# Optimization experiments

Hardware: AMD Instinct MI355X
Metric: run time of the kernel (lower is better)

Reference implementation:

```python
import jax, jax.numpy as jnp
import numpy as np

B, S, D = 2, 4096, 2048
H = 16
DN, DR = 128, 64          # qk_nope_head_dim, qk_rope_head_dim
DQK = DN + DR             # 192
DV = 128                  # v_head_dim
QL, KVL = 512, 512        # q_lora_rank, kv_lora_rank
L = 64                    # block_len
SCALE = DQK ** -0.5
ROPE_THETA = 10000.0


def rms_norm(x, w, eps=1e-6):
    x = x.astype(jnp.float32)
    return x * jax.lax.rsqrt(jnp.mean(x * x, axis=-1, keepdims=True) + eps) * w


def apply_rope(x, cos, sin):
    # x: [b, s, h, d]; cos/sin: [s, d//2]; pairs are consecutive (view(-1,2))
    shp = x.shape
    x2 = x.reshape(shp[:-1] + (-1, 2))
    xr, xi = x2[..., 0], x2[..., 1]
    c = cos[None, :, None, :]
    s_ = sin[None, :, None, :]
    yr = xr * c - xi * s_
    yi = xr * s_ + xi * c
    return jnp.stack([yr, yi], axis=-1).reshape(shp)


def ssa(q, k, v, init_state):
    # chunked causal linear attention; q,k: [b,s,h,dk], v: [b,s,h,dv]
    b, s, h, dk = q.shape
    dv = v.shape[-1]
    nc = s // L
    qc = q.reshape(b, nc, L, h, dk)
    kc = k.reshape(b, nc, L, h, dk)
    vc = v.reshape(b, nc, L, h, dv)
    # per-chunk k^T v outer products -> [b,c,h,dk,dv]
    kv = jnp.einsum('bclhk,bclhv->bchkv', kc, vc)
    cs = jnp.cumsum(kv, axis=1)
    # exclusive prefix (state at chunk start) + initial state
    states = jnp.concatenate([jnp.zeros_like(cs[:, :1]), cs[:, :-1]], axis=1) + init_state[:, None]
    inter = jnp.einsum('bclhk,bchkv->bclhv', qc, states)
    sc = jnp.einsum('bclhk,bcmhk->bchlm', qc, kc)
    mask = jnp.tril(jnp.ones((L, L), dtype=bool))
    sc = jnp.where(mask, sc, 0.0)
    intra = jnp.einsum('bchlm,bcmhv->bclhv', sc, vc)
    return (inter + intra).reshape(b, s, h, dv)


def setup_inputs() -> dict:
    key = jax.random.key(0)
    ks = jax.random.split(key, 8)
    x = jax.random.normal(ks[0], (B, S, D), dtype=jnp.float32)
    # rope tables for qk_rope_head_dim
    inv = 1.0 / (ROPE_THETA ** (np.arange(0, DR, 2, dtype=np.float32) / DR))
    ang = np.outer(np.arange(S, dtype=np.float32), inv)
    cos = jnp.asarray(np.cos(ang), dtype=jnp.float32)
    sin = jnp.asarray(np.sin(ang), dtype=jnp.float32)
    std = 0.02
    wq_a = jax.random.normal(ks[1], (QL, D), dtype=jnp.float32) * std
    wq_b = jax.random.normal(ks[2], (H * DQK, QL), dtype=jnp.float32) * std
    wkv_a = jax.random.normal(ks[3], (KVL + DR, D), dtype=jnp.float32) * std
    wkv_b = jax.random.normal(ks[4], (H * (DN + DV), KVL), dtype=jnp.float32) * std
    wo = jax.random.normal(ks[5], (D, H * DV), dtype=jnp.float32) * std
    q_norm_w = jnp.ones((QL,), dtype=jnp.float32)
    kv_norm_w = jnp.ones((KVL,), dtype=jnp.float32)
    init_state = jnp.zeros((B, H, DQK, DV), dtype=jnp.float32)
    return {"x": x, "start_pos": 0, "cos": cos, "sin": sin,
            "wq_a": wq_a, "wq_b": wq_b, "wkv_a": wkv_a, "wkv_b": wkv_b,
            "wo": wo, "q_norm_w": q_norm_w, "kv_norm_w": kv_norm_w,
            "init_state": init_state}


def reference(x, start_pos, cos, sin, wq_a, wq_b, wkv_a, wkv_b, wo,
              q_norm_w, kv_norm_w, init_state):
    b, s, _ = x.shape
    q = rms_norm(x @ wq_a.T, q_norm_w) @ wq_b.T
    q = q.reshape(b, s, H, DQK)
    q_nope, q_pe = q[..., :DN], q[..., DN:]
    q_pe = apply_rope(q_pe, cos, sin)
    kvp = x @ wkv_a.T
    kv_lat, k_pe = kvp[..., :KVL], kvp[..., KVL:]
    k_pe = apply_rope(k_pe[:, :, None, :], cos, sin)  # [b,s,1,DR]
    kv = rms_norm(kv_lat, kv_norm_w) @ wkv_b.T
    kv = kv.reshape(b, s, H, DN + DV)
    k_nope, v = kv[..., :DN], kv[..., DN:]
    q = jnp.concatenate([q_nope, q_pe], axis=-1)
    k = jnp.concatenate([k_nope, jnp.broadcast_to(k_pe, (b, s, H, DR))], axis=-1)
    q = jax.nn.elu(q) + 1.0
    k = jax.nn.elu(k) + 1.0
    out = ssa(q, k, v, init_state) * SCALE
    out = out.reshape(b, s, H * DV) @ wo.T
    return out
```

## Files before the change

kernel.cpp:

```cpp
#include <hip/hip_runtime.h>

static __device__ __align__(256) unsigned char g_ws[645200000];

typedef __attribute__((ext_vector_type(8))) __bf16 bf16x8;
typedef __attribute__((ext_vector_type(4))) float  f32x4;
typedef __attribute__((ext_vector_type(8))) unsigned short u16x8;

__device__ __forceinline__ short f2bf(float f) {
    union { float f; unsigned u; } v; v.f = f;
    unsigned r = v.u + 0x7FFFu + ((v.u >> 16) & 1u);
    return (short)(r >> 16);
}
__device__ __forceinline__ float bf2f(unsigned short u) {
    union { unsigned u; float f; } v; v.u = ((unsigned)u) << 16;
    return v.f;
}
__device__ __forceinline__ float elu1(float x) {
    return x > 0.f ? x + 1.f : __expf(x);
}
__device__ __forceinline__ void gload_lds16(const void* g, void* l) {
    __builtin_amdgcn_global_load_lds(
        (const __attribute__((address_space(1))) unsigned int*)g,
        (__attribute__((address_space(3))) unsigned int*)l, 16, 0, 0);
}

#define MFMA16(a, b, c) __builtin_amdgcn_mfma_f32_16x16x32_bf16((a), (b), (c), 0, 0, 0)

__global__ __launch_bounds__(256) void cvt_bf16(
    const float* __restrict__ src, short* __restrict__ dst, int n)
{
    const int i = (blockIdx.x * 256 + threadIdx.x) * 4;
    if (i < n) {
        const float4 v = *(const float4*)(src + i);
        ushort4 o;
        o.x = (unsigned short)f2bf(v.x);
        o.y = (unsigned short)f2bf(v.y);
        o.z = (unsigned short)f2bf(v.z);
        o.w = (unsigned short)f2bf(v.w);
        *(ushort4*)(dst + i) = o;
    }
}

template <int EPI>
__global__ __launch_bounds__(512, 2) void gemm256(
    const short* __restrict__ A, int lda,
    const short* __restrict__ Bt, int ldb,
    void* __restrict__ C0, void* __restrict__ C1, int ldc,
    int Nvalid, int K, int nbx,
    const float* __restrict__ cosT, const float* __restrict__ sinT)
{
    __shared__ char ldsB[131072];
    const int t = threadIdx.x;
    const int lane = t & 63, w = t >> 6;

    const int cpx = gridDim.x >> 3;
    const int id = (blockIdx.x & 7) * cpx + (blockIdx.x >> 3);
    const int row0 = (id % nbx) * 256;
    const int col0 = (id / nbx) * 256;

    const int r8 = lane >> 3;
    const int srcb = (((lane & 7) ^ r8) << 4);
    const char* aSrc = (const char*)A + ((size_t)(row0 + w * 32 + r8) * lda) * 2 + srcb;
    const char* bSrc = (const char*)Bt + ((size_t)(col0 + w * 32 + r8) * ldb) * 2 + srcb;
    const size_t aRow8 = (size_t)lda * 16;
    const size_t bRow8 = (size_t)ldb * 16;
    char* aDst = ldsB + w * 4096 + lane * 16;
    char* bDst = ldsB + 65536 + w * 4096 + lane * 16;

    const int wr = (w >> 2) * 128, wc = (w & 3) * 64;
    const int l15 = lane & 15;
    const int g16 = (lane >> 4) * 16;
    const int rxor = (l15 & 7) << 4;

    const int NT = K >> 6;

    auto STAGE = [&](int j) {
        const int sb = (j & 1) * 32768;
        const size_t kb = (size_t)j * 128;
#pragma unroll
        for (int p = 0; p < 4; ++p) {
            gload_lds16(aSrc + kb + p * aRow8, aDst + sb + p * 1024);
            gload_lds16(bSrc + kb + p * bRow8, bDst + sb + p * 1024);
        }
    };

    f32x4 acc[8][4];
#pragma unroll
    for (int i = 0; i < 8; ++i)
#pragma unroll
        for (int j = 0; j < 4; ++j) acc[i][j] = (f32x4){0.f, 0.f, 0.f, 0.f};

    STAGE(0); STAGE(1);

#pragma unroll 1
    for (int kt = 0; kt < NT; ++kt) {
        if (kt + 1 < NT) asm volatile("s_waitcnt vmcnt(8)" ::: "memory");
        else             asm volatile("s_waitcnt vmcnt(0)" ::: "memory");
        __builtin_amdgcn_s_barrier();
        __builtin_amdgcn_sched_barrier(0);
        const char* aS = ldsB + (kt & 1) * 32768;
        const char* bS = ldsB + 65536 + (kt & 1) * 32768;
        bf16x8 af[8], bf4[4];
#pragma unroll
        for (int i = 0; i < 8; ++i)
            af[i] = *(const bf16x8*)(aS + (wr + i * 16 + l15) * 128 + (g16 ^ rxor));
#pragma unroll
        for (int j = 0; j < 4; ++j)
            bf4[j] = *(const bf16x8*)(bS + (wc + j * 16 + l15) * 128 + (g16 ^ rxor));
        asm volatile("s_waitcnt lgkmcnt(0)" ::: "memory");
        __builtin_amdgcn_sched_barrier(0);
        __builtin_amdgcn_s_setprio(1);
#pragma unroll
        for (int i = 0; i < 8; ++i)
#pragma unroll
            for (int j = 0; j < 4; ++j)
                acc[i][j] = MFMA16(af[i], bf4[j], acc[i][j]);
        __builtin_amdgcn_s_setprio(0);
#pragma unroll
        for (int i = 0; i < 8; ++i)
            af[i] = *(const bf16x8*)(aS + (wr + i * 16 + l15) * 128 + ((64 + g16) ^ rxor));
#pragma unroll
        for (int j = 0; j < 4; ++j)
            bf4[j] = *(const bf16x8*)(bS + (wc + j * 16 + l15) * 128 + ((64 + g16) ^ rxor));
        asm volatile("s_waitcnt lgkmcnt(0)" ::: "memory");
        __builtin_amdgcn_sched_barrier(0);
        __builtin_amdgcn_s_barrier();
        if (kt + 2 < NT) STAGE(kt + 2);
        __builtin_amdgcn_s_setprio(1);
#pragma unroll
        for (int i = 0; i < 8; ++i)
#pragma unroll
            for (int j = 0; j < 4; ++j)
                acc[i][j] = MFMA16(af[i], bf4[j], acc[i][j]);
        __builtin_amdgcn_s_setprio(0);
    }

    const int rbase = (lane >> 4) * 4;
#pragma unroll
    for (int i = 0; i < 8; ++i)
#pragma unroll
        for (int j = 0; j < 4; ++j) {
            const int cc = col0 + wc + j * 16 + l15;
            if (EPI <= 1) {
                if (cc < Nvalid) {
#pragma unroll
                    for (int q = 0; q < 4; ++q) {
                        const size_t o = (size_t)(row0 + wr + i * 16 + rbase + q) * ldc + cc;
                        if (EPI == 1) ((short*)C0)[o] = f2bf(acc[i][j][q]);
                        else          ((float*)C0)[o] = acc[i][j][q];
                    }
                }
            } else if (EPI == 2) {
                const int hh = cc / 192, d = cc - hh * 192;
#pragma unroll
                for (int q = 0; q < 4; ++q) {
                    const int row = row0 + wr + i * 16 + rbase + q;
                    const int s = row & 4095, b = row >> 12;
                    const float v = acc[i][j][q];
                    const float pv = __shfl_xor(v, 1, 64);
                    float val;
                    if (d >= 128) {
                        const int p = (d - 128) >> 1;
                        const float c = cosT[(size_t)s * 32 + p];
                        const float si = sinT[(size_t)s * 32 + p];
                        val = ((d & 1) == 0) ? (v * c - pv * si) : (pv * si + v * c);
                    } else val = v;
                    ((short*)C0)[((size_t)(b * 16 + hh) * 4096 + s) * 192 + d] = f2bf(elu1(val));
                }
            } else {
                const int hh = cc >> 8, d = cc & 255;
#pragma unroll
                for (int q = 0; q < 4; ++q) {
                    const int row = row0 + wr + i * 16 + rbase + q;
                    const int s = row & 4095, b = row >> 12;
                    const float v = acc[i][j][q];
                    if (d < 128)
                        ((short*)C0)[((size_t)(b * 16 + hh) * 4096 + s) * 192 + d] = f2bf(elu1(v));
                    else
                        ((short*)C1)[((size_t)(b * 16 + hh) * 4096 + s) * 128 + d - 128] = f2bf(v);
                }
            }
        }
}

__global__ __launch_bounds__(256) void rms_rope(
    const short* __restrict__ Y1,
    const float* __restrict__ qw, const float* __restrict__ kvw,
    const float* __restrict__ cosT, const float* __restrict__ sinT,
    short* __restrict__ qn, short* __restrict__ kvn, short* __restrict__ kpe)
{
    __shared__ float red[256];
    const int row = blockIdx.x;
    const int s = row & 4095;
    const int t = threadIdx.x;
    const unsigned short* yr = (const unsigned short*)(Y1 + (size_t)row * 1088);

    float v0 = bf2f(yr[t]), v1 = bf2f(yr[t + 256]);
    red[t] = v0 * v0 + v1 * v1;
    __syncthreads();
    for (int off = 128; off > 0; off >>= 1) {
        if (t < off) red[t] += red[t + off];
        __syncthreads();
    }
    float rs = rsqrtf(red[0] / 512.f + 1e-6f);
    __syncthreads();
    qn[(size_t)row * 512 + t]       = f2bf(v0 * rs * qw[t]);
    qn[(size_t)row * 512 + t + 256] = f2bf(v1 * rs * qw[t + 256]);

    float u0 = bf2f(yr[512 + t]), u1 = bf2f(yr[768 + t]);
    red[t] = u0 * u0 + u1 * u1;
    __syncthreads();
    for (int off = 128; off > 0; off >>= 1) {
        if (t < off) red[t] += red[t + off];
        __syncthreads();
    }
    float rs2 = rsqrtf(red[0] / 512.f + 1e-6f);
    kvn[(size_t)row * 512 + t]       = f2bf(u0 * rs2 * kvw[t]);
    kvn[(size_t)row * 512 + t + 256] = f2bf(u1 * rs2 * kvw[t + 256]);

    if (t < 32) {
        float xr = bf2f(yr[1024 + 2 * t]), xi = bf2f(yr[1024 + 2 * t + 1]);
        float cc = cosT[(size_t)s * 32 + t], sn = sinT[(size_t)s * 32 + t];
        kpe[(size_t)row * 64 + 2 * t]     = f2bf(elu1(xr * cc - xi * sn));
        kpe[(size_t)row * 64 + 2 * t + 1] = f2bf(elu1(xr * sn + xi * cc));
    }
}

__global__ __launch_bounds__(256) void build_kpe(
    const short* __restrict__ kpe, short* __restrict__ k_ssa)
{
    const int row = blockIdx.x;
    const int s = row & 4095, b = row >> 12;
    const int t = threadIdx.x;
    const short* pe = kpe + (size_t)row * 64;
#pragma unroll
    for (int it = 0; it < 4; ++it) {
        const int idx = t + it * 256;
        const int h = idx >> 6, dd = idx & 63;
        k_ssa[((size_t)(b * 16 + h) * 4096 + s) * 192 + 128 + dd] = pe[dd];
    }
}

__global__ __launch_bounds__(256) void init_t_kern(
    const float* __restrict__ init, float* __restrict__ initT)
{
    __shared__ float tile[32][33];
    const int bh = blockIdx.y;
    const int tk = blockIdx.x % 6, tv = blockIdx.x / 6;
    const int r0 = threadIdx.x >> 5, c = threadIdx.x & 31;
    const float* src = init + (size_t)bh * 24576;
    float* dst = initT + (size_t)bh * 24576;
#pragma unroll
    for (int p = 0; p < 4; ++p) {
        const int rr = r0 + 8 * p;
        tile[rr][c] = src[(size_t)(tk * 32 + rr) * 128 + tv * 32 + c];
    }
    __syncthreads();
#pragma unroll
    for (int p = 0; p < 4; ++p) {
        const int rr = r0 + 8 * p;
        dst[(size_t)(tv * 32 + rr) * 192 + tk * 32 + c] = tile[c][rr];
    }
}

__global__ __launch_bounds__(256, 3) void ssa_kv(
    const short* __restrict__ k_ssa, const short* __restrict__ v_ssa,
    short* __restrict__ kvcT)
{
    __shared__ short smem[25600];
    short (*lkt)[72] = (short(*)[72])smem;
    short (*lvt)[72] = (short(*)[72])(smem + 192 * 72);
    short (*outT)[200] = (short(*)[200])smem;
    const int c = blockIdx.x, h = blockIdx.y, b = blockIdx.z;
    const int bh = b * 16 + h;
    const short* Kc = k_ssa + ((size_t)bh * 4096 + c * 64) * 192;
    const short* Vc = v_ssa + ((size_t)bh * 4096 + c * 64) * 128;
    const int t = threadIdx.x, lane = t & 63, w = t >> 6;
    const int l15 = lane & 15, kg = (lane >> 4) * 8, rbase = (lane >> 4) * 4;

    for (int i = t; i < 64 * 48; i += 256) {
        const int row = i / 48, c4 = (i % 48) * 4;
        ushort4 kv4 = *(const ushort4*)(Kc + (size_t)row * 192 + c4);
        lkt[c4 + 0][row] = (short)kv4.x;
        lkt[c4 + 1][row] = (short)kv4.y;
        lkt[c4 + 2][row] = (short)kv4.z;
        lkt[c4 + 3][row] = (short)kv4.w;
    }
    for (int i = t; i < 64 * 32; i += 256) {
        const int row = i >> 5, c4 = (i & 31) * 4;
        ushort4 vv = *(const ushort4*)(Vc + (size_t)row * 128 + c4);
        lvt[c4 + 0][row] = (short)vv.x;
        lvt[c4 + 1][row] = (short)vv.y;
        lvt[c4 + 2][row] = (short)vv.z;
        lvt[c4 + 3][row] = (short)vv.w;
    }
    __syncthreads();

    f32x4 acc[2][12];
#pragma unroll
    for (int i = 0; i < 2; ++i)
#pragma unroll
        for (int j = 0; j < 12; ++j) acc[i][j] = (f32x4){0.f, 0.f, 0.f, 0.f};
#pragma unroll
    for (int ks = 0; ks < 2; ++ks) {
        bf16x8 af[2];
#pragma unroll
        for (int i = 0; i < 2; ++i) af[i] = *(const bf16x8*)&lvt[w * 32 + i * 16 + l15][ks * 32 + kg];
#pragma unroll
        for (int j = 0; j < 12; ++j) {
            const bf16x8 bk = *(const bf16x8*)&lkt[j * 16 + l15][ks * 32 + kg];
#pragma unroll
            for (int i = 0; i < 2; ++i) acc[i][j] = MFMA16(af[i], bk, acc[i][j]);
        }
    }
    __syncthreads();
#pragma unroll
    for (int i = 0; i < 2; ++i)
#pragma unroll
        for (int j = 0; j < 12; ++j)
#pragma unroll
            for (int q = 0; q < 4; ++q)
                outT[w * 32 + i * 16 + rbase + q][j * 16 + l15] = f2bf(acc[i][j][q]);
    __syncthreads();

    short* kvp = kvcT + ((size_t)bh * 64 + c) * 24576;
    for (int i = t; i < 3072; i += 256) {
        const int s8 = i * 8;
        const int row = s8 / 192, col = s8 % 192;
        *(u16x8*)(kvp + s8) = *(const u16x8*)&outT[row][col];
    }
}

__global__ __launch_bounds__(256) void ssa_scan(
    short* __restrict__ kvc, const float* __restrict__ initT)
{
    const int bh = blockIdx.y;
    const int e8 = (blockIdx.x * 256 + threadIdx.x) * 8;
    float st[8];
    {
        const float4 i0 = *(const float4*)(initT + (size_t)bh * 24576 + e8);
        const float4 i1 = *(const float4*)(initT + (size_t)bh * 24576 + e8 + 4);
        st[0] = i0.x; st[1] = i0.y; st[2] = i0.z; st[3] = i0.w;
        st[4] = i1.x; st[5] = i1.y; st[6] = i1.z; st[7] = i1.w;
    }
    short* p = kvc + (size_t)bh * 64 * 24576 + e8;
    for (int cc = 0; cc < 64; ++cc) {
        const u16x8 v = *(const u16x8*)p;
        u16x8 o;
#pragma unroll
        for (int j = 0; j < 8; ++j) o[j] = (unsigned short)f2bf(st[j]);
        *(u16x8*)p = o;
#pragma unroll
        for (int j = 0; j < 8; ++j) st[j] += bf2f(v[j]);
        p += 24576;
    }
}

__global__ __launch_bounds__(256, 2) void ssa_out(
    const short* __restrict__ q_ssa, const short* __restrict__ k_ssa,
    const short* __restrict__ v_ssa, const short* __restrict__ states,
    short* __restrict__ attnb)
{
    __shared__ short lk[64][200];
    __shared__ short lvt[128][72];
    __shared__ short lst[128][104];
    __shared__ short lsc[64][72];
    const int c = blockIdx.x, h = blockIdx.y, b = blockIdx.z;
    const int bh = b * 16 + h;
    const short* Qb = q_ssa + ((size_t)bh * 4096 + c * 64) * 192;
    const short* Kc = k_ssa + ((size_t)bh * 4096 + c * 64) * 192;
    const short* Vc = v_ssa + ((size_t)bh * 4096 + c * 64) * 128;
    const short* st = states + ((size_t)bh * 64 + c) * 24576;
    const int t = threadIdx.x, lane = t & 63, w = t >> 6;
    const int l15 = lane & 15, kg = (lane >> 4) * 8, rbase = (lane >> 4) * 4;

    bf16x8 aq[6];
    {
        const short* Qr = Qb + (size_t)(w * 16 + l15) * 192 + kg;
#pragma unroll
        for (int ks = 0; ks < 6; ++ks) aq[ks] = *(const bf16x8*)(Qr + ks * 32);
    }
    for (int i = t; i < 1536; i += 256) {
        const int row = i / 24, c8 = (i % 24) * 8;
        *(u16x8*)&lk[row][c8] = *(const u16x8*)(Kc + (size_t)row * 192 + c8);
    }
    for (int i = t; i < 2048; i += 256) {
        const int row = i >> 5, c4 = (i & 31) * 4;
        ushort4 vv = *(const ushort4*)(Vc + (size_t)row * 128 + c4);
        lvt[c4 + 0][row] = (short)vv.x;
        lvt[c4 + 1][row] = (short)vv.y;
        lvt[c4 + 2][row] = (short)vv.z;
        lvt[c4 + 3][row] = (short)vv.w;
    }
    for (int i = t; i < 1536; i += 256) {
        const int row = i / 12, c8 = (i % 12) * 8;
        *(u16x8*)&lst[row][c8] = *(const u16x8*)(st + (size_t)row * 192 + c8);
    }
    __syncthreads();

    {
        f32x4 sc[4];
#pragma unroll
        for (int j = 0; j < 4; ++j) sc[j] = (f32x4){0.f, 0.f, 0.f, 0.f};
#pragma unroll
        for (int ks = 0; ks < 6; ++ks)
#pragma unroll
            for (int j = 0; j < 4; ++j) {
                const bf16x8 bk = *(const bf16x8*)&lk[j * 16 + l15][ks * 32 + kg];
                sc[j] = MFMA16(aq[ks], bk, sc[j]);
            }
#pragma unroll
        for (int j = 0; j < 4; ++j)
#pragma unroll
            for (int q = 0; q < 4; ++q) {
                const int l = w * 16 + rbase + q;
                const int m = j * 16 + l15;
                lsc[l][m] = f2bf((m <= l) ? sc[j][q] : 0.f);
            }
    }
    __syncthreads();

    f32x4 acc[8];
#pragma unroll
    for (int j = 0; j < 8; ++j) acc[j] = (f32x4){0.f, 0.f, 0.f, 0.f};
#pragma unroll
    for (int ks = 0; ks < 2; ++ks) {
        const bf16x8 as = *(const bf16x8*)&lsc[w * 16 + l15][ks * 32 + kg];
#pragma unroll
        for (int j = 0; j < 8; ++j) {
            const bf16x8 bv = *(const bf16x8*)&lvt[j * 16 + l15][ks * 32 + kg];
            acc[j] = MFMA16(as, bv, acc[j]);
        }
    }
#pragma unroll
    for (int ks = 0; ks < 3; ++ks)
#pragma unroll
        for (int j = 0; j < 8; ++j) {
            const bf16x8 bs = *(const bf16x8*)&lst[j * 16 + l15][ks * 32 + kg];
            acc[j] = MFMA16(aq[ks], bs, acc[j]);
        }
    __syncthreads();
    for (int i = t; i < 1536; i += 256) {
        const int row = i / 12, c8 = (i % 12) * 8;
        *(u16x8*)&lst[row][c8] = *(const u16x8*)(st + (size_t)row * 192 + 96 + c8);
    }
    __syncthreads();
#pragma unroll
    for (int ks = 3; ks < 6; ++ks)
#pragma unroll
        for (int j = 0; j < 8; ++j) {
            const bf16x8 bs = *(const bf16x8*)&lst[j * 16 + l15][(ks - 3) * 32 + kg];
            acc[j] = MFMA16(aq[ks], bs, acc[j]);
        }

    const float scale = 0.07216878364870322f;
#pragma unroll
    for (int j = 0; j < 8; ++j)
#pragma unroll
        for (int q = 0; q < 4; ++q) {
            const int l = w * 16 + rbase + q;
            const int dv = j * 16 + l15;
            attnb[((size_t)(b * 4096 + c * 64 + l)) * 2048 + h * 128 + dv] = f2bf(acc[j][q] * scale);
        }
}

extern "C" void kernel_launch(void* const* d_in, const int* in_sizes, int n_in,
                              void* d_out, int out_size, void* d_ws, size_t ws_size,
                              hipStream_t stream) {
    const float* x     = (const float*)d_in[0];
    const float* cosT  = (const float*)d_in[2];
    const float* sinT  = (const float*)d_in[3];
    const float* wq_a  = (const float*)d_in[4];
    const float* wq_b  = (const float*)d_in[5];
    const float* wkv_a = (const float*)d_in[6];
    const float* wkv_b = (const float*)d_in[7];
    const float* wo    = (const float*)d_in[8];
    const float* qw    = (const float*)d_in[9];
    const float* kvw   = (const float*)d_in[10];
    const float* init  = (const float*)d_in[11];
    float* out = (float*)d_out;

    void* base = nullptr;
    hipGetSymbolAddress(&base, HIP_SYMBOL(g_ws));
    char* ws = (char*)base;
    size_t off = 0;
    auto take = [&](size_t bytes) -> char* {
        char* p = ws + off;
        off += (bytes + 255) & ~(size_t)255;
        return p;
    };
    short* xb    = (short*)take((size_t)8192 * 2048 * 2);
    short* wab   = (short*)take((size_t)1280 * 2048 * 2);
    short* wqbb  = (short*)take((size_t)3072 * 512 * 2);
    short* wkvbb = (short*)take((size_t)4096 * 512 * 2);
    short* wob   = (short*)take((size_t)2048 * 2048 * 2);
    short* y1b   = (short*)take((size_t)8192 * 1088 * 2);
    short* qnb   = (short*)take((size_t)8192 * 512 * 2);
    short* kvnb  = (short*)take((size_t)8192 * 512 * 2);
    short* kpe   = (short*)take((size_t)8192 * 64 * 2);
    short* qs    = (short*)take((size_t)2 * 16 * 4096 * 192 * 2);
    short* ksb   = (short*)take((size_t)2 * 16 * 4096 * 192 * 2);
    short* vsb   = (short*)take((size_t)2 * 16 * 4096 * 128 * 2);
    short* kvcT  = (short*)take((size_t)2048 * 24576 * 2);
    float* initT = (float*)take((size_t)32 * 24576 * 4);
    short* attnb = (short*)take((size_t)8192 * 2048 * 2);

    cvt_bf16<<<(8192 * 2048 / 4 + 255) / 256, 256, 0, stream>>>(x, xb, 8192 * 2048);
    cvt_bf16<<<(512 * 2048 / 4 + 255) / 256, 256, 0, stream>>>(wq_a, wab, 512 * 2048);
    cvt_bf16<<<(576 * 2048 / 4 + 255) / 256, 256, 0, stream>>>(wkv_a, wab + (size_t)512 * 2048, 576 * 2048);
    hipMemsetAsync(wab + (size_t)1088 * 2048, 0, (size_t)192 * 2048 * 2, stream);
    cvt_bf16<<<(3072 * 512 / 4 + 255) / 256, 256, 0, stream>>>(wq_b, wqbb, 3072 * 512);
    cvt_bf16<<<(4096 * 512 / 4 + 255) / 256, 256, 0, stream>>>(wkv_b, wkvbb, 4096 * 512);
    cvt_bf16<<<(2048 * 2048 / 4 + 255) / 256, 256, 0, stream>>>(wo, wob, 2048 * 2048);
    init_t_kern<<<dim3(24, 32), 256, 0, stream>>>(init, initT);

    gemm256<1><<<160, 512, 0, stream>>>(xb, 2048, wab, 2048, y1b, nullptr, 1088, 1088, 2048, 32, nullptr, nullptr);
    rms_rope<<<8192, 256, 0, stream>>>(y1b, qw, kvw, cosT, sinT, qnb, kvnb, kpe);
    gemm256<2><<<384, 512, 0, stream>>>(qnb, 512, wqbb, 512, qs, nullptr, 0, 3072, 512, 32, cosT, sinT);
    gemm256<3><<<512, 512, 0, stream>>>(kvnb, 512, wkvbb, 512, ksb, vsb, 0, 4096, 512, 32, nullptr, nullptr);
    build_kpe<<<8192, 256, 0, stream>>>(kpe, ksb);
    ssa_kv<<<dim3(64, 16, 2), 256, 0, stream>>>(ksb, vsb, kvcT);
    ssa_scan<<<dim3(12, 32), 256, 0, stream>>>(kvcT, initT);
    ssa_out<<<dim3(64, 16, 2), 256, 0, stream>>>(qs, ksb, vsb, kvcT, attnb);
    gemm256<0><<<256, 512, 0, stream>>>(attnb, 2048, wob, 2048, out, nullptr, 2048, 2048, 2048, 32, nullptr, nullptr);
}
```

Before: 623.2 us.

## Switch GEMMs to 256x128 tiles with triple-buffered LDS and a single barrier per k-step

The shared GEMM kernel now uses 256x128 output tiles instead of 256x256, doubling the grid size for every projection. Each wave now computes a 64x64 sub-tile. The LDS pipeline goes from double to triple buffering, so only one barrier per k-iteration is needed, and the next-next stage is issued before the compute. This is meant to improve CU fill on small GEMMs and reduce barrier stalls, at the cost of lower arithmetic intensity per tile, more LDS use (about 144KB), and occupancy of one block per CU.

Result: slower. 648.3 us (+4.0%).

```diff
diff --git a/kernel.cpp b/kernel.cpp
--- a/kernel.cpp
+++ b/kernel.cpp
@@ -42,32 +42,32 @@
 }
 
 template <int EPI>
-__global__ __launch_bounds__(512, 2) void gemm256(
+__global__ __launch_bounds__(512, 1) void gemm_bn(
     const short* __restrict__ A, int lda,
     const short* __restrict__ Bt, int ldb,
     void* __restrict__ C0, void* __restrict__ C1, int ldc,
-    int Nvalid, int K, int nbx,
+    int Nvalid, int K, int nby,
     const float* __restrict__ cosT, const float* __restrict__ sinT)
 {
-    __shared__ char ldsB[131072];
+    __shared__ char lds[147456];
     const int t = threadIdx.x;
     const int lane = t & 63, w = t >> 6;
 
     const int cpx = gridDim.x >> 3;
-    const int id = (blockIdx.x & 7) * cpx + (blockIdx.x >> 3);
-    const int row0 = (id % nbx) * 256;
-    const int col0 = (id / nbx) * 256;
+    const int id = ((int)blockIdx.x & 7) * cpx + ((int)blockIdx.x >> 3);
+    const int col0 = (id % nby) * 128;
+    const int row0 = (id / nby) * 256;
 
     const int r8 = lane >> 3;
-    const int srcb = (((lane & 7) ^ r8) << 4);
+    const int srcb = ((lane & 7) ^ r8) << 4;
     const char* aSrc = (const char*)A + ((size_t)(row0 + w * 32 + r8) * lda) * 2 + srcb;
-    const char* bSrc = (const char*)Bt + ((size_t)(col0 + w * 32 + r8) * ldb) * 2 + srcb;
+    const char* bSrc = (const char*)Bt + ((size_t)(col0 + w * 16 + r8) * ldb) * 2 + srcb;
     const size_t aRow8 = (size_t)lda * 16;
     const size_t bRow8 = (size_t)ldb * 16;
-    char* aDst = ldsB + w * 4096 + lane * 16;
-    char* bDst = ldsB + 65536 + w * 4096 + lane * 16;
-
-    const int wr = (w >> 2) * 128, wc = (w & 3) * 64;
+    char* aD = lds + w * 4096 + lane * 16;
+    char* bD = lds + 98304 + w * 2048 + lane * 16;
+
+    const int wr = (w >> 1) * 64, wc = (w & 1) * 64;
     const int l15 = lane & 15;
     const int g16 = (lane >> 4) * 16;
     const int rxor = (l15 & 7) << 4;
@@ -75,18 +75,19 @@
     const int NT = K >> 6;
 
     auto STAGE = [&](int j) {
-        const int sb = (j & 1) * 32768;
+        const int sl = j % 3;
         const size_t kb = (size_t)j * 128;
 #pragma unroll
-        for (int p = 0; p < 4; ++p) {
-            gload_lds16(aSrc + kb + p * aRow8, aDst + sb + p * 1024);
-            gload_lds16(bSrc + kb + p * bRow8, bDst + sb + p * 1024);
-        }
+        for (int p = 0; p < 4; ++p)
+            gload_lds16(aSrc + kb + p * aRow8, aD + sl * 32768 + p * 1024);
+#pragma unroll
+        for (int p = 0; p < 2; ++p)
+            gload_lds16(bSrc + kb + p * bRow8, bD + sl * 16384 + p * 1024);
     };
 
-    f32x4 acc[8][4];
-#pragma unroll
-    for (int i = 0; i < 8; ++i)
+    f32x4 acc[4][4];
+#pragma unroll
+    for (int i = 0; i < 4; ++i)
 #pragma unroll
         for (int j = 0; j < 4; ++j) acc[i][j] = (f32x4){0.f, 0.f, 0.f, 0.f};
 
@@ -94,50 +95,36 @@
 
 #pragma unroll 1
     for (int kt = 0; kt < NT; ++kt) {
-        if (kt + 1 < NT) asm volatile("s_waitcnt vmcnt(8)" ::: "memory");
+        if (kt + 1 < NT) asm volatile("s_waitcnt vmcnt(6)" ::: "memory");
         else             asm volatile("s_waitcnt vmcnt(0)" ::: "memory");
-        __builtin_amdgcn_s_barrier();
-        __builtin_amdgcn_sched_barrier(0);
-        const char* aS = ldsB + (kt & 1) * 32768;
-        const char* bS = ldsB + 65536 + (kt & 1) * 32768;
-        bf16x8 af[8], bf4[4];
-#pragma unroll
-        for (int i = 0; i < 8; ++i)
-            af[i] = *(const bf16x8*)(aS + (wr + i * 16 + l15) * 128 + (g16 ^ rxor));
-#pragma unroll
-        for (int j = 0; j < 4; ++j)
-            bf4[j] = *(const bf16x8*)(bS + (wc + j * 16 + l15) * 128 + (g16 ^ rxor));
-        asm volatile("s_waitcnt lgkmcnt(0)" ::: "memory");
-        __builtin_amdgcn_sched_barrier(0);
-        __builtin_amdgcn_s_setprio(1);
-#pragma unroll
-        for (int i = 0; i < 8; ++i)
-#pragma unroll
-            for (int j = 0; j < 4; ++j)
-                acc[i][j] = MFMA16(af[i], bf4[j], acc[i][j]);
-        __builtin_amdgcn_s_setprio(0);
-#pragma unroll
-        for (int i = 0; i < 8; ++i)
-            af[i] = *(const bf16x8*)(aS + (wr + i * 16 + l15) * 128 + ((64 + g16) ^ rxor));
-#pragma unroll
-        for (int j = 0; j < 4; ++j)
-            bf4[j] = *(const bf16x8*)(bS + (wc + j * 16 + l15) * 128 + ((64 + g16) ^ rxor));
-        asm volatile("s_waitcnt lgkmcnt(0)" ::: "memory");
         __builtin_amdgcn_sched_barrier(0);
         __builtin_amdgcn_s_barrier();
         if (kt + 2 < NT) STAGE(kt + 2);
-        __builtin_amdgcn_s_setprio(1);
-#pragma unroll
-        for (int i = 0; i < 8; ++i)
+        const char* aS = lds + (kt % 3) * 32768;
+        const char* bS = lds + 98304 + (kt % 3) * 16384;
+#pragma unroll
+        for (int half = 0; half < 2; ++half) {
+            const int ko = half * 64;
+            bf16x8 af[4], bf4[4];
+#pragma unroll
+            for (int i = 0; i < 4; ++i)
+                af[i] = *(const bf16x8*)(aS + (wr + i * 16 + l15) * 128 + ((ko + g16) ^ rxor));
 #pragma unroll
             for (int j = 0; j < 4; ++j)
-                acc[i][j] = MFMA16(af[i], bf4[j], acc[i][j]);
-        __builtin_amdgcn_s_setprio(0);
+                bf4[j] = *(const bf16x8*)(bS + (wc + j * 16 + l15) * 128 + ((ko + g16) ^ rxor));
+            __builtin_amdgcn_s_setprio(1);
+#pragma unroll
+            for (int i = 0; i < 4; ++i)
+#pragma unroll
+                for (int j = 0; j < 4; ++j)
+                    acc[i][j] = MFMA16(af[i], bf4[j], acc[i][j]);
+            __builtin_amdgcn_s_setprio(0);
+        }
     }
 
     const int rbase = (lane >> 4) * 4;
 #pragma unroll
-    for (int i = 0; i < 8; ++i)
+    for (int i = 0; i < 4; ++i)
 #pragma unroll
         for (int j = 0; j < 4; ++j) {
             const int cc = col0 + wc + j * 16 + l15;
@@ -514,13 +501,13 @@
     cvt_bf16<<<(2048 * 2048 / 4 + 255) / 256, 256, 0, stream>>>(wo, wob, 2048 * 2048);
     init_t_kern<<<dim3(24, 32), 256, 0, stream>>>(init, initT);
 
-    gemm256<1><<<160, 512, 0, stream>>>(xb, 2048, wab, 2048, y1b, nullptr, 1088, 1088, 2048, 32, nullptr, nullptr);
+    gemm_bn<1><<<320, 512, 0, stream>>>(xb, 2048, wab, 2048, y1b, nullptr, 1088, 1088, 2048, 10, nullptr, nullptr);
     rms_rope<<<8192, 256, 0, stream>>>(y1b, qw, kvw, cosT, sinT, qnb, kvnb, kpe);
-    gemm256<2><<<384, 512, 0, stream>>>(qnb, 512, wqbb, 512, qs, nullptr, 0, 3072, 512, 32, cosT, sinT);
-    gemm256<3><<<512, 512, 0, stream>>>(kvnb, 512, wkvbb, 512, ksb, vsb, 0, 4096, 512, 32, nullptr, nullptr);
+    gemm_bn<2><<<768, 512, 0, stream>>>(qnb, 512, wqbb, 512, qs, nullptr, 0, 3072, 512, 24, cosT, sinT);
+    gemm_bn<3><<<1024, 512, 0, stream>>>(kvnb, 512, wkvbb, 512, ksb, vsb, 0, 4096, 512, 32, nullptr, nullptr);
     build_kpe<<<8192, 256, 0, stream>>>(kpe, ksb);
     ssa_kv<<<dim3(64, 16, 2), 256, 0, stream>>>(ksb, vsb, kvcT);
     ssa_scan<<<dim3(12, 32), 256, 0, stream>>>(kvcT, initT);
     ssa_out<<<dim3(64, 16, 2), 256, 0, stream>>>(qs, ksb, vsb, kvcT, attnb);
-    gemm256<0><<<256, 512, 0, stream>>>(attnb, 2048, wob, 2048, out, nullptr, 2048, 2048, 2048, 32, nullptr, nullptr);
-}
+    gemm_bn<0><<<512, 512, 0, stream>>>(attnb, 2048, wob, 2048, out, nullptr, 2048, 2048, 2048, 16, nullptr, nullptr);
+}
```
